# Performance work log

Measured on AMD Instinct MI355X. Metric: run time of the kernel, lower is better.

Reference implementation:

```python
import jax, jax.numpy as jnp
import numpy as np

NEG_BIG = -1e10
LEAKY_ALPHA = 0.2

def setup_inputs() -> dict:
    key = jax.random.key(0)
    k1, k2, k3, k4 = jax.random.split(key, 4)
    B, N, F, H = 8, 2048, 128, 4
    X = jax.random.normal(k1, (B, N, F), dtype=jnp.float32)
    A = jax.random.bernoulli(k2, 0.06, (B, N, N)).astype(jnp.float32)
    A = jnp.maximum(A, jnp.eye(N, dtype=jnp.float32)[None])
    attn_self = jax.random.normal(k3, (H, F), dtype=jnp.float32) * 0.1
    attn_neigh = jax.random.normal(k4, (H, F), dtype=jnp.float32) * 0.1
    return {"X": X, "A": A, "attn_self": attn_self, "attn_neigh": attn_neigh}

def reference(X, A, attn_self, attn_neigh):
    # mode 0, concat reduction, tanh activation (applied per head, as in call_mode0)
    B, N, F = X.shape
    H = attn_self.shape[0]
    a_self = jnp.einsum('bnf,hf->bhn', X, attn_self)   # [B,H,N]
    a_neigh = jnp.einsum('bnf,hf->bhn', X, attn_neigh)  # [B,H,N]
    dense = a_self[:, :, :, None] + a_neigh[:, :, None, :]  # [B,H,N,N]
    dense = jnp.where(dense >= 0, dense, LEAKY_ALPHA * dense)  # leaky relu 0.2
    mask = jnp.where(A == 0.0, NEG_BIG, 0.0)[:, None, :, :]   # [B,1,N,N]
    attn = jax.nn.softmax(dense + mask, axis=-1)               # [B,H,N,N]
    feats = jnp.einsum('bhnm,bmf->bhnf', attn, X)              # [B,H,N,F]
    feats = jnp.tanh(feats)
    # concat heads on feature axis -> [B,N,H*F]
    return feats.transpose(0, 2, 1, 3).reshape(B, N, H * F)
```

## Files before the change

### kernel.cpp

```cpp
#include <hip/hip_runtime.h>
#include <hip/hip_bf16.h>
#include <math.h>

#define N_NODES 2048
#define F_DIM   128
#define H_HEADS 4
#define B_BATCH 8
#define LEAKY   0.2f

typedef float f32x4 __attribute__((ext_vector_type(4)));
typedef float f32x2 __attribute__((ext_vector_type(2)));

__device__ __forceinline__ float tanh_fast(float x) {
    const float e = __expf(2.0f * x);
    return 1.0f - 2.0f / (e + 1.0f);
}

__global__ __launch_bounds__(256) void gat_proj(const float* __restrict__ X,
                                                const float* __restrict__ wS,
                                                const float* __restrict__ wN,
                                                float* __restrict__ aSt,
                                                float* __restrict__ aNt) {
    const int wave = threadIdx.x >> 6;
    const int lane = threadIdx.x & 63;
    const int row  = blockIdx.x * 4 + wave;
    const float* xr = X + (size_t)row * F_DIM;
    const float x0 = xr[lane];
    const float x1 = xr[lane + 64];
    float4 ps4, pn4;
    float* psv = (float*)&ps4;
    float* pnv = (float*)&pn4;
#pragma unroll
    for (int h = 0; h < H_HEADS; ++h) {
        float ps = x0 * wS[h * F_DIM + lane] + x1 * wS[h * F_DIM + 64 + lane];
        float pn = x0 * wN[h * F_DIM + lane] + x1 * wN[h * F_DIM + 64 + lane];
#pragma unroll
        for (int off = 32; off > 0; off >>= 1) {
            ps += __shfl_xor(ps, off);
            pn += __shfl_xor(pn, off);
        }
        psv[h] = ps;
        pnv[h] = pn;
    }
    if (lane == 0) {
        ((float4*)aSt)[row] = ps4;
        ((float4*)aNt)[row] = pn4;
    }
}

__global__ __launch_bounds__(256) void gat_gmax(const float* __restrict__ aNt,
                                                float* __restrict__ gmax) {
    const int b = blockIdx.x;
    const int tid = threadIdx.x;
    const int lane = tid & 63;
    const int wv = tid >> 6;
    __shared__ float4 s_part[4];
    float4 m = make_float4(-1e30f, -1e30f, -1e30f, -1e30f);
    const float4* src = (const float4*)aNt + (size_t)b * N_NODES;
    for (int n = tid; n < N_NODES; n += 256) {
        const float4 v = src[n];
        m.x = fmaxf(m.x, v.x); m.y = fmaxf(m.y, v.y);
        m.z = fmaxf(m.z, v.z); m.w = fmaxf(m.w, v.w);
    }
#pragma unroll
    for (int off = 32; off > 0; off >>= 1) {
        m.x = fmaxf(m.x, __shfl_xor(m.x, off));
        m.y = fmaxf(m.y, __shfl_xor(m.y, off));
        m.z = fmaxf(m.z, __shfl_xor(m.z, off));
        m.w = fmaxf(m.w, __shfl_xor(m.w, off));
    }
    if (lane == 0) s_part[wv] = m;
    __syncthreads();
    if (tid == 0) {
        float4 r = s_part[0];
#pragma unroll
        for (int w = 1; w < 4; ++w) {
            r.x = fmaxf(r.x, s_part[w].x); r.y = fmaxf(r.y, s_part[w].y);
            r.z = fmaxf(r.z, s_part[w].z); r.w = fmaxf(r.w, s_part[w].w);
        }
        ((float4*)gmax)[b] = r;
    }
}

#define FMA16(PV, XV)                                        \
    do {                                                     \
        acc[0][0] = fmaf((PV).x, (XV).x, acc[0][0]);         \
        acc[0][1] = fmaf((PV).x, (XV).y, acc[0][1]);         \
        acc[0][2] = fmaf((PV).x, (XV).z, acc[0][2]);         \
        acc[0][3] = fmaf((PV).x, (XV).w, acc[0][3]);         \
        acc[1][0] = fmaf((PV).y, (XV).x, acc[1][0]);         \
        acc[1][1] = fmaf((PV).y, (XV).y, acc[1][1]);         \
        acc[1][2] = fmaf((PV).y, (XV).z, acc[1][2]);         \
        acc[1][3] = fmaf((PV).y, (XV).w, acc[1][3]);         \
        acc[2][0] = fmaf((PV).z, (XV).x, acc[2][0]);         \
        acc[2][1] = fmaf((PV).z, (XV).y, acc[2][1]);         \
        acc[2][2] = fmaf((PV).z, (XV).z, acc[2][2]);         \
        acc[2][3] = fmaf((PV).z, (XV).w, acc[2][3]);         \
        acc[3][0] = fmaf((PV).w, (XV).x, acc[3][0]);         \
        acc[3][1] = fmaf((PV).w, (XV).y, acc[3][1]);         \
        acc[3][2] = fmaf((PV).w, (XV).z, acc[3][2]);         \
        acc[3][3] = fmaf((PV).w, (XV).w, acc[3][3]);         \
    } while (0)

__global__ __launch_bounds__(256, 6) void gat_main(const float* __restrict__ X,
                                                   const float* __restrict__ A,
                                                   const float* __restrict__ aSt,
                                                   const float* __restrict__ aNt,
                                                   const float* __restrict__ gmax,
                                                   float* __restrict__ out) {
    const int tid = threadIdx.x;
    const int bid = blockIdx.x;
    const int row = ((bid & 7) << 11) | (bid >> 3);
    const int b = row >> 11;
    const int lane = tid & 63;
    const int wv = tid >> 6;

    __shared__ short  s_idx[N_NODES];
    __shared__ float4 s_p4[256];
    __shared__ int    s_off[256];
    __shared__ float  s_red[4 * 512];
    __shared__ int    s_wtot[4];
    __shared__ float  s_M[4];
    __shared__ float  s_sv[4];
    __shared__ float  s_scr[16];

    const f32x4* Arow = (const f32x4*)(A + (size_t)row * N_NODES);
    const f32x4 a0 = __builtin_nontemporal_load(Arow + tid * 2);
    const f32x4 a1 = __builtin_nontemporal_load(Arow + tid * 2 + 1);

    if (tid < 4) {
        const float sv = aSt[(size_t)row * 4 + tid];
        const float g = gmax[b * 4 + tid];
        float v = sv + g;
        v = fmaxf(v, LEAKY * v);
        s_M[tid] = v;
        s_sv[tid] = sv;
    }

    const float av[8] = {a0.x, a0.y, a0.z, a0.w, a1.x, a1.y, a1.z, a1.w};
    int c = 0;
#pragma unroll
    for (int k = 0; k < 8; ++k) c += (av[k] != 0.0f) ? 1 : 0;

    int incl = c;
#pragma unroll
    for (int d = 1; d < 64; d <<= 1) {
        const int u = __shfl_up(incl, d);
        if (lane >= d) incl += u;
    }
    if (lane == 63) s_wtot[wv] = incl;
    __syncthreads();
    int wbase = 0;
#pragma unroll
    for (int w = 0; w < 4; ++w) wbase += (w < wv) ? s_wtot[w] : 0;
    const int cnt = s_wtot[0] + s_wtot[1] + s_wtot[2] + s_wtot[3];
    int pos = wbase + (incl - c);
#pragma unroll
    for (int k = 0; k < 8; ++k) {
        if (av[k] != 0.0f) s_idx[pos++] = (short)(tid * 8 + k);
    }
    __syncthreads();

    float acc[4][4];
#pragma unroll
    for (int h = 0; h < 4; ++h)
#pragma unroll
        for (int fi = 0; fi < 4; ++fi) acc[h][fi] = 0.0f;
    float lsum[4] = {0.0f, 0.0f, 0.0f, 0.0f};

    const int jsub = tid >> 5;
    const int f4 = tid & 31;
    const char* XbB = (const char*)(X + (size_t)b * N_NODES * F_DIM) + (f4 << 4);
    const float4* aNb4 = (const float4*)aNt + (size_t)b * N_NODES;

    for (int base = 0; base < cnt; base += 256) {
        const int clen = min(256, cnt - base);
        if (tid < clen) {
            const int m = s_idx[base + tid];
            const float4 t = aNb4[m];
            const float tv[4] = {t.x, t.y, t.z, t.w};
            float4 p4;
            float* pp = (float*)&p4;
#pragma unroll
            for (int h = 0; h < H_HEADS; ++h) {
                float v = s_sv[h] + tv[h];
                v = fmaxf(v, LEAKY * v);
                const float p = __expf(v - s_M[h]);
                pp[h] = p;
                lsum[h] += p;
            }
            s_p4[tid] = p4;
            s_off[tid] = m << 9;
        }
        __syncthreads();
#pragma unroll 4
        for (int j = jsub; j < clen; j += 8) {
            const float4 pv = s_p4[j];
            const float4 xv = *(const float4*)(XbB + (unsigned)s_off[j]);
            FMA16(pv, xv);
        }
        __syncthreads();
    }

#pragma unroll
    for (int h = 0; h < H_HEADS; ++h) {
        float v = lsum[h];
#pragma unroll
        for (int off = 32; off > 0; off >>= 1) v += __shfl_xor(v, off);
        if (lane == 0) s_scr[wv * 4 + h] = v;
    }
#pragma unroll
    for (int h = 0; h < 4; ++h)
#pragma unroll
        for (int fi = 0; fi < 4; ++fi)
            acc[h][fi] += __shfl_xor(acc[h][fi], 32);
    if (lane < 32) {
        float4* red4 = (float4*)s_red;
#pragma unroll
        for (int h = 0; h < 4; ++h)
            red4[wv * 128 + h * 32 + f4] =
                make_float4(acc[h][0], acc[h][1], acc[h][2], acc[h][3]);
    }
    __syncthreads();

    const int hf = tid * 2;
    const int h = tid >> 6;
    const float l = s_scr[h] + s_scr[4 + h] + s_scr[8 + h] + s_scr[12 + h];
    const float invl = 1.0f / l;
    float v0 = 0.0f, v1 = 0.0f;
#pragma unroll
    for (int w = 0; w < 4; ++w) {
        v0 += s_red[w * 512 + hf];
        v1 += s_red[w * 512 + hf + 1];
    }
    f32x2 o;
    o.x = tanh_fast(v0 * invl);
    o.y = tanh_fast(v1 * invl);
    __builtin_nontemporal_store(o, (f32x2*)&out[(size_t)row * 512 + hf]);
}

extern "C" void kernel_launch(void* const* d_in, const int* in_sizes, int n_in,
                              void* d_out, int out_size, void* d_ws, size_t ws_size,
                              hipStream_t stream) {
    const float* X  = (const float*)d_in[0];
    const float* A  = (const float*)d_in[1];
    const float* wS = (const float*)d_in[2];
    const float* wN = (const float*)d_in[3];
    float* out = (float*)d_out;

    float* aSt = (float*)d_ws;
    float* aNt = aSt + (size_t)B_BATCH * N_NODES * H_HEADS;
    float* gmx = aNt + (size_t)B_BATCH * N_NODES * H_HEADS;

    gat_proj<<<(B_BATCH * N_NODES) / 4, 256, 0, stream>>>(X, wS, wN, aSt, aNt);
    gat_gmax<<<B_BATCH, 256, 0, stream>>>(aNt, gmx);
    gat_main<<<B_BATCH * N_NODES, 256, 0, stream>>>(X, A, aSt, aNt, gmx, out);
}
```

Before: 102.8 us.

## Bit-pack adjacency in a separate pass and compact indices from bitmask in main kernel

Adds a pre-pass that reads the float adjacency and writes a 1-bit-per-edge mask into workspace. The main kernel then reads 256 bytes of mask per row instead of 8 KB of floats, and one wave builds the neighbor index list with popcount, a scan and a find-first-set loop. The pass still reads the whole of A once, so it mainly moves the A read out of the main kernel and adds a launch plus extra mask traffic. A fallback keeps the old kernel when the workspace is too small.

Measured after the change: 111.3 us. 1.08x slower.

```diff
diff --git a/kernel.cpp b/kernel.cpp
--- a/kernel.cpp
+++ b/kernel.cpp
@@ -14,6 +14,25 @@
 __device__ __forceinline__ float tanh_fast(float x) {
     const float e = __expf(2.0f * x);
     return 1.0f - 2.0f / (e + 1.0f);
+}
+
+__global__ __launch_bounds__(256) void gat_bitpack(const float* __restrict__ A,
+                                                   unsigned char* __restrict__ maskb) {
+    const int row = blockIdx.x;
+    const int tid = threadIdx.x;
+    const f32x4* Ar = (const f32x4*)(A + (size_t)row * N_NODES);
+    const f32x4 a0 = __builtin_nontemporal_load(Ar + tid * 2);
+    const f32x4 a1 = __builtin_nontemporal_load(Ar + tid * 2 + 1);
+    unsigned b = 0;
+    b |= (a0.x != 0.0f ? 1u : 0u) << 0;
+    b |= (a0.y != 0.0f ? 1u : 0u) << 1;
+    b |= (a0.z != 0.0f ? 1u : 0u) << 2;
+    b |= (a0.w != 0.0f ? 1u : 0u) << 3;
+    b |= (a1.x != 0.0f ? 1u : 0u) << 4;
+    b |= (a1.y != 0.0f ? 1u : 0u) << 5;
+    b |= (a1.z != 0.0f ? 1u : 0u) << 6;
+    b |= (a1.w != 0.0f ? 1u : 0u) << 7;
+    maskb[(size_t)row * 256 + tid] = (unsigned char)b;
 }
 
 __global__ __launch_bounds__(256) void gat_proj(const float* __restrict__ X,
@@ -103,7 +122,7 @@
     } while (0)
 
 __global__ __launch_bounds__(256, 6) void gat_main(const float* __restrict__ X,
-                                                   const float* __restrict__ A,
+                                                   const unsigned* __restrict__ maskw,
                                                    const float* __restrict__ aSt,
                                                    const float* __restrict__ aNt,
                                                    const float* __restrict__ gmax,
@@ -119,47 +138,43 @@
     __shared__ float4 s_p4[256];
     __shared__ int    s_off[256];
     __shared__ float  s_red[4 * 512];
-    __shared__ int    s_wtot[4];
     __shared__ float  s_M[4];
     __shared__ float  s_sv[4];
     __shared__ float  s_scr[16];
-
-    const f32x4* Arow = (const f32x4*)(A + (size_t)row * N_NODES);
-    const f32x4 a0 = __builtin_nontemporal_load(Arow + tid * 2);
-    const f32x4 a1 = __builtin_nontemporal_load(Arow + tid * 2 + 1);
-
-    if (tid < 4) {
-        const float sv = aSt[(size_t)row * 4 + tid];
-        const float g = gmax[b * 4 + tid];
+    __shared__ int    s_cnt;
+
+    unsigned mw = 0;
+    if (tid < 64) mw = maskw[(size_t)row * 64 + tid];
+
+    if (tid >= 64 && tid < 68) {
+        const int t = tid - 64;
+        const float sv = aSt[(size_t)row * 4 + t];
+        const float g = gmax[b * 4 + t];
         float v = sv + g;
         v = fmaxf(v, LEAKY * v);
-        s_M[tid] = v;
-        s_sv[tid] = sv;
-    }
-
-    const float av[8] = {a0.x, a0.y, a0.z, a0.w, a1.x, a1.y, a1.z, a1.w};
-    int c = 0;
-#pragma unroll
-    for (int k = 0; k < 8; ++k) c += (av[k] != 0.0f) ? 1 : 0;
-
-    int incl = c;
-#pragma unroll
-    for (int d = 1; d < 64; d <<= 1) {
-        const int u = __shfl_up(incl, d);
-        if (lane >= d) incl += u;
-    }
-    if (lane == 63) s_wtot[wv] = incl;
-    __syncthreads();
-    int wbase = 0;
-#pragma unroll
-    for (int w = 0; w < 4; ++w) wbase += (w < wv) ? s_wtot[w] : 0;
-    const int cnt = s_wtot[0] + s_wtot[1] + s_wtot[2] + s_wtot[3];
-    int pos = wbase + (incl - c);
-#pragma unroll
-    for (int k = 0; k < 8; ++k) {
-        if (av[k] != 0.0f) s_idx[pos++] = (short)(tid * 8 + k);
-    }
-    __syncthreads();
+        s_M[t] = v;
+        s_sv[t] = sv;
+    }
+
+    if (tid < 64) {
+        const int c = __popc(mw);
+        int incl = c;
+#pragma unroll
+        for (int d = 1; d < 64; d <<= 1) {
+            const int u = __shfl_up(incl, d);
+            if (lane >= d) incl += u;
+        }
+        if (lane == 63) s_cnt = incl;
+        int p = incl - c;
+        unsigned m = mw;
+        while (m) {
+            const int bpos = __ffs(m) - 1;
+            s_idx[p++] = (short)((lane << 5) + bpos);
+            m &= m - 1;
+        }
+    }
+    __syncthreads();
+    const int cnt = s_cnt;
 
     float acc[4][4];
 #pragma unroll
@@ -239,6 +254,143 @@
     __builtin_nontemporal_store(o, (f32x2*)&out[(size_t)row * 512 + hf]);
 }
 
+__global__ __launch_bounds__(256, 6) void gat_main_fb(const float* __restrict__ X,
+                                                      const float* __restrict__ A,
+                                                      const float* __restrict__ aSt,
+                                                      const float* __restrict__ aNt,
+                                                      const float* __restrict__ gmax,
+                                                      float* __restrict__ out) {
+    const int tid = threadIdx.x;
+    const int bid = blockIdx.x;
+    const int row = ((bid & 7) << 11) | (bid >> 3);
+    const int b = row >> 11;
+    const int lane = tid & 63;
+    const int wv = tid >> 6;
+
+    __shared__ short  s_idx[N_NODES];
+    __shared__ float4 s_p4[256];
+    __shared__ int    s_off[256];
+    __shared__ float  s_red[4 * 512];
+    __shared__ int    s_wtot[4];
+    __shared__ float  s_M[4];
+    __shared__ float  s_sv[4];
+    __shared__ float  s_scr[16];
+
+    const f32x4* Arow = (const f32x4*)(A + (size_t)row * N_NODES);
+    const f32x4 a0 = __builtin_nontemporal_load(Arow + tid * 2);
+    const f32x4 a1 = __builtin_nontemporal_load(Arow + tid * 2 + 1);
+
+    if (tid < 4) {
+        const float sv = aSt[(size_t)row * 4 + tid];
+        const float g = gmax[b * 4 + tid];
+        float v = sv + g;
+        v = fmaxf(v, LEAKY * v);
+        s_M[tid] = v;
+        s_sv[tid] = sv;
+    }
+
+    const float av[8] = {a0.x, a0.y, a0.z, a0.w, a1.x, a1.y, a1.z, a1.w};
+    int c = 0;
+#pragma unroll
+    for (int k = 0; k < 8; ++k) c += (av[k] != 0.0f) ? 1 : 0;
+
+    int incl = c;
+#pragma unroll
+    for (int d = 1; d < 64; d <<= 1) {
+        const int u = __shfl_up(incl, d);
+        if (lane >= d) incl += u;
+    }
+    if (lane == 63) s_wtot[wv] = incl;
+    __syncthreads();
+    int wbase = 0;
+#pragma unroll
+    for (int w = 0; w < 4; ++w) wbase += (w < wv) ? s_wtot[w] : 0;
+    const int cnt = s_wtot[0] + s_wtot[1] + s_wtot[2] + s_wtot[3];
+    int pos = wbase + (incl - c);
+#pragma unroll
+    for (int k = 0; k < 8; ++k) {
+        if (av[k] != 0.0f) s_idx[pos++] = (short)(tid * 8 + k);
+    }
+    __syncthreads();
+
+    float acc[4][4];
+#pragma unroll
+    for (int h = 0; h < 4; ++h)
+#pragma unroll
+        for (int fi = 0; fi < 4; ++fi) acc[h][fi] = 0.0f;
+    float lsum[4] = {0.0f, 0.0f, 0.0f, 0.0f};
+
+    const int jsub = tid >> 5;
+    const int f4 = tid & 31;
+    const char* XbB = (const char*)(X + (size_t)b * N_NODES * F_DIM) + (f4 << 4);
+    const float4* aNb4 = (const float4*)aNt + (size_t)b * N_NODES;
+
+    for (int base = 0; base < cnt; base += 256) {
+        const int clen = min(256, cnt - base);
+        if (tid < clen) {
+            const int m = s_idx[base + tid];
+            const float4 t = aNb4[m];
+            const float tv[4] = {t.x, t.y, t.z, t.w};
+            float4 p4;
+            float* pp = (float*)&p4;
+#pragma unroll
+            for (int h = 0; h < H_HEADS; ++h) {
+                float v = s_sv[h] + tv[h];
+                v = fmaxf(v, LEAKY * v);
+                const float p = __expf(v - s_M[h]);
+                pp[h] = p;
+                lsum[h] += p;
+            }
+            s_p4[tid] = p4;
+            s_off[tid] = m << 9;
+        }
+        __syncthreads();
+#pragma unroll 4
+        for (int j = jsub; j < clen; j += 8) {
+            const float4 pv = s_p4[j];
+            const float4 xv = *(const float4*)(XbB + (unsigned)s_off[j]);
+            FMA16(pv, xv);
+        }
+        __syncthreads();
+    }
+
+#pragma unroll
+    for (int h = 0; h < H_HEADS; ++h) {
+        float v = lsum[h];
+#pragma unroll
+        for (int off = 32; off > 0; off >>= 1) v += __shfl_xor(v, off);
+        if (lane == 0) s_scr[wv * 4 + h] = v;
+    }
+#pragma unroll
+    for (int h = 0; h < 4; ++h)
+#pragma unroll
+        for (int fi = 0; fi < 4; ++fi)
+            acc[h][fi] += __shfl_xor(acc[h][fi], 32);
+    if (lane < 32) {
+        float4* red4 = (float4*)s_red;
+#pragma unroll
+        for (int h = 0; h < 4; ++h)
+            red4[wv * 128 + h * 32 + f4] =
+                make_float4(acc[h][0], acc[h][1], acc[h][2], acc[h][3]);
+    }
+    __syncthreads();
+
+    const int hf = tid * 2;
+    const int h = tid >> 6;
+    const float l = s_scr[h] + s_scr[4 + h] + s_scr[8 + h] + s_scr[12 + h];
+    const float invl = 1.0f / l;
+    float v0 = 0.0f, v1 = 0.0f;
+#pragma unroll
+    for (int w = 0; w < 4; ++w) {
+        v0 += s_red[w * 512 + hf];
+        v1 += s_red[w * 512 + hf + 1];
+    }
+    f32x2 o;
+    o.x = tanh_fast(v0 * invl);
+    o.y = tanh_fast(v1 * invl);
+    __builtin_nontemporal_store(o, (f32x2*)&out[(size_t)row * 512 + hf]);
+}
+
 extern "C" void kernel_launch(void* const* d_in, const int* in_sizes, int n_in,
                               void* d_out, int out_size, void* d_ws, size_t ws_size,
                               hipStream_t stream) {
@@ -251,8 +403,18 @@
     float* aSt = (float*)d_ws;
     float* aNt = aSt + (size_t)B_BATCH * N_NODES * H_HEADS;
     float* gmx = aNt + (size_t)B_BATCH * N_NODES * H_HEADS;
+    unsigned char* maskb = (unsigned char*)(gmx + B_BATCH * H_HEADS);
+
+    const size_t need = ((size_t)B_BATCH * N_NODES * H_HEADS * 2 + B_BATCH * H_HEADS) * 4
+                        + (size_t)B_BATCH * N_NODES * (N_NODES / 8);
 
     gat_proj<<<(B_BATCH * N_NODES) / 4, 256, 0, stream>>>(X, wS, wN, aSt, aNt);
     gat_gmax<<<B_BATCH, 256, 0, stream>>>(aNt, gmx);
-    gat_main<<<B_BATCH * N_NODES, 256, 0, stream>>>(X, A, aSt, aNt, gmx, out);
-}
+    if (ws_size >= need) {
+        gat_bitpack<<<B_BATCH * N_NODES, 256, 0, stream>>>(A, maskb);
+        gat_main<<<B_BATCH * N_NODES, 256, 0, stream>>>(X, (const unsigned*)maskb,
+                                                        aSt, aNt, gmx, out);
+    } else {
+        gat_main_fb<<<B_BATCH * N_NODES, 256, 0, stream>>>(X, A, aSt, aNt, gmx, out);
+    }
+}
```

## Replace sparse gather aggregation with dense bf16 split-precision MFMA kernel

Applied to the files above, without the earlier changes.

Adds a transpose kernel that splits X into bf16 hi/lo parts in a feature-major layout. A new dense kernel computes masked softmax weights for 32 rows by 4 heads per block and runs the attention-times-X product on MFMA 16x16x32 bf16, using hi and lo passes to keep accuracy close to fp32, with double-buffered LDS staging. This replaces the per-row compaction and scalar FMA gather with dense matrix-core work over all N columns, which skips the gather and compaction overhead but computes on zero entries too. The probabilities are rounded to bf16, which adds some error, and the old path stays as a fallback when the workspace is too small.

After: 187.2 us. 1.82x slower.

```diff
diff --git a/kernel.cpp b/kernel.cpp
--- a/kernel.cpp
+++ b/kernel.cpp
@@ -10,17 +10,28 @@
 
 typedef float f32x4 __attribute__((ext_vector_type(4)));
 typedef float f32x2 __attribute__((ext_vector_type(2)));
+typedef short bf16x8 __attribute__((ext_vector_type(8)));
+typedef float f32x4a __attribute__((ext_vector_type(4)));
 
 __device__ __forceinline__ float tanh_fast(float x) {
     const float e = __expf(2.0f * x);
     return 1.0f - 2.0f / (e + 1.0f);
+}
+__device__ __forceinline__ unsigned short f2bf(float x) {
+    unsigned u = __float_as_uint(x);
+    u += 0x7FFFu + ((u >> 16) & 1u);
+    return (unsigned short)(u >> 16);
+}
+__device__ __forceinline__ float bf2f(unsigned short s) {
+    return __uint_as_float(((unsigned)s) << 16);
 }
 
 __global__ __launch_bounds__(256) void gat_proj(const float* __restrict__ X,
                                                 const float* __restrict__ wS,
                                                 const float* __restrict__ wN,
                                                 float* __restrict__ aSt,
-                                                float* __restrict__ aNt) {
+                                                float* __restrict__ aNt,
+                                                float* __restrict__ aNp) {
     const int wave = threadIdx.x >> 6;
     const int lane = threadIdx.x & 63;
     const int row  = blockIdx.x * 4 + wave;
@@ -45,6 +56,10 @@
     if (lane == 0) {
         ((float4*)aSt)[row] = ps4;
         ((float4*)aNt)[row] = pn4;
+        const int bb = row >> 11, nn = row & (N_NODES - 1);
+#pragma unroll
+        for (int h = 0; h < H_HEADS; ++h)
+            aNp[((size_t)(bb * H_HEADS + h)) * N_NODES + nn] = pnv[h];
     }
 }
 
@@ -82,32 +97,172 @@
     }
 }
 
-#define FMA16(PV, XV)                                        \
-    do {                                                     \
-        acc[0][0] = fmaf((PV).x, (XV).x, acc[0][0]);         \
-        acc[0][1] = fmaf((PV).x, (XV).y, acc[0][1]);         \
-        acc[0][2] = fmaf((PV).x, (XV).z, acc[0][2]);         \
-        acc[0][3] = fmaf((PV).x, (XV).w, acc[0][3]);         \
-        acc[1][0] = fmaf((PV).y, (XV).x, acc[1][0]);         \
-        acc[1][1] = fmaf((PV).y, (XV).y, acc[1][1]);         \
-        acc[1][2] = fmaf((PV).y, (XV).z, acc[1][2]);         \
-        acc[1][3] = fmaf((PV).y, (XV).w, acc[1][3]);         \
-        acc[2][0] = fmaf((PV).z, (XV).x, acc[2][0]);         \
-        acc[2][1] = fmaf((PV).z, (XV).y, acc[2][1]);         \
-        acc[2][2] = fmaf((PV).z, (XV).z, acc[2][2]);         \
-        acc[2][3] = fmaf((PV).z, (XV).w, acc[2][3]);         \
-        acc[3][0] = fmaf((PV).w, (XV).x, acc[3][0]);         \
-        acc[3][1] = fmaf((PV).w, (XV).y, acc[3][1]);         \
-        acc[3][2] = fmaf((PV).w, (XV).z, acc[3][2]);         \
-        acc[3][3] = fmaf((PV).w, (XV).w, acc[3][3]);         \
-    } while (0)
-
-__global__ __launch_bounds__(256, 6) void gat_main(const float* __restrict__ X,
-                                                   const float* __restrict__ A,
-                                                   const float* __restrict__ aSt,
-                                                   const float* __restrict__ aNt,
-                                                   const float* __restrict__ gmax,
-                                                   float* __restrict__ out) {
+__global__ __launch_bounds__(256) void gat_xtpose(const float* __restrict__ X,
+                                                  unsigned short* __restrict__ XThi,
+                                                  unsigned short* __restrict__ XTlo) {
+    const int bb = blockIdx.x & 7;
+    const int K0 = (blockIdx.x >> 3) << 7;
+    const int tid = threadIdx.x;
+    __shared__ unsigned short ht[128][136];
+    __shared__ unsigned short lt[128][136];
+    const int f4 = (tid & 31) * 4;
+    for (int kk = tid >> 5; kk < 128; kk += 8) {
+        const float4 x = *(const float4*)&X[((size_t)(bb * N_NODES + K0 + kk)) * F_DIM + f4];
+        const float xs[4] = {x.x, x.y, x.z, x.w};
+#pragma unroll
+        for (int q = 0; q < 4; ++q) {
+            const unsigned short hi = f2bf(xs[q]);
+            ht[f4 + q][kk] = hi;
+            lt[f4 + q][kk] = f2bf(xs[q] - bf2f(hi));
+        }
+    }
+    __syncthreads();
+    const int f = tid >> 1, hf = tid & 1;
+    const size_t obase = ((size_t)(bb * F_DIM + f)) * N_NODES + K0 + hf * 64;
+#pragma unroll
+    for (int c = 0; c < 64; c += 8) {
+        *(bf16x8*)&XThi[obase + c] = *(const bf16x8*)&ht[f][hf * 64 + c];
+        *(bf16x8*)&XTlo[obase + c] = *(const bf16x8*)&lt[f][hf * 64 + c];
+    }
+}
+
+__global__ __launch_bounds__(256, 2) void gat_dense(const float* __restrict__ A,
+                                                    const float* __restrict__ aSt,
+                                                    const float* __restrict__ aNp,
+                                                    const float* __restrict__ gmax,
+                                                    const unsigned short* __restrict__ XThi,
+                                                    const unsigned short* __restrict__ XTlo,
+                                                    float* __restrict__ out) {
+    const int tid = threadIdx.x;
+    const int bid = blockIdx.x;
+    const int b = bid & 7;
+    const int Rbase = (bid >> 3) << 5;
+    const int h = tid >> 6;
+    const int lane = tid & 63;
+    const int mrow = lane & 15;
+    const int kch = lane >> 4;
+
+    __shared__ unsigned short ldsXhi[2][128 * 40];
+    __shared__ unsigned short ldsXlo[2][128 * 40];
+    __shared__ float sml[128];
+
+    const int row0 = b * N_NODES + Rbase + mrow;
+    const float g  = gmax[b * 4 + h];
+    const float aS0 = aSt[(size_t)row0 * 4 + h];
+    const float aS1 = aSt[(size_t)(row0 + 16) * 4 + h];
+    float m0 = aS0 + g; m0 = fmaxf(m0, LEAKY * m0);
+    float m1 = aS1 + g; m1 = fmaxf(m1, LEAKY * m1);
+
+    const float* Ar0 = A + (size_t)row0 * N_NODES;
+    const float* Ar1 = Ar0 + (size_t)16 * N_NODES;
+    const float* aNh = aNp + ((size_t)(b * H_HEADS + h)) * N_NODES;
+
+    const int sf = tid >> 1, shf = tid & 1;
+    const unsigned short* XThiB = XThi + ((size_t)(b * F_DIM + sf)) * N_NODES + shf * 16;
+    const unsigned short* XTloB = XTlo + ((size_t)(b * F_DIM + sf)) * N_NODES + shf * 16;
+    const int sdst = sf * 40 + shf * 16;
+
+    f32x4a acc0[8], acc1[8];
+#pragma unroll
+    for (int ft = 0; ft < 8; ++ft) {
+        acc0[ft] = (f32x4a){0.f, 0.f, 0.f, 0.f};
+        acc1[ft] = (f32x4a){0.f, 0.f, 0.f, 0.f};
+    }
+    float ls0 = 0.f, ls1 = 0.f;
+
+    bf16x8 rh0 = *(const bf16x8*)(XThiB);
+    bf16x8 rh1 = *(const bf16x8*)(XThiB + 8);
+    bf16x8 rl0 = *(const bf16x8*)(XTloB);
+    bf16x8 rl1 = *(const bf16x8*)(XTloB + 8);
+    *(bf16x8*)&ldsXhi[0][sdst] = rh0; *(bf16x8*)&ldsXhi[0][sdst + 8] = rh1;
+    *(bf16x8*)&ldsXlo[0][sdst] = rl0; *(bf16x8*)&ldsXlo[0][sdst + 8] = rl1;
+    __syncthreads();
+
+    const int NS = N_NODES / 32;
+    for (int s = 0; s < NS; ++s) {
+        const int cur = s & 1;
+        const int T = s << 5;
+        if (s + 1 < NS) {
+            const int Tn = T + 32;
+            rh0 = *(const bf16x8*)(XThiB + Tn);
+            rh1 = *(const bf16x8*)(XThiB + Tn + 8);
+            rl0 = *(const bf16x8*)(XTloB + Tn);
+            rl1 = *(const bf16x8*)(XTloB + Tn + 8);
+        }
+        const int ko = T + kch * 8;
+        const f32x4 a0a = __builtin_nontemporal_load((const f32x4*)(Ar0 + ko));
+        const f32x4 a0b = __builtin_nontemporal_load((const f32x4*)(Ar0 + ko + 4));
+        const f32x4 a1a = __builtin_nontemporal_load((const f32x4*)(Ar1 + ko));
+        const f32x4 a1b = __builtin_nontemporal_load((const f32x4*)(Ar1 + ko + 4));
+        const f32x4 ana = *(const f32x4*)(aNh + ko);
+        const f32x4 anb = *(const f32x4*)(aNh + ko + 4);
+        const float a0v[8] = {a0a.x, a0a.y, a0a.z, a0a.w, a0b.x, a0b.y, a0b.z, a0b.w};
+        const float a1v[8] = {a1a.x, a1a.y, a1a.z, a1a.w, a1b.x, a1b.y, a1b.z, a1b.w};
+        const float anv[8] = {ana.x, ana.y, ana.z, ana.w, anb.x, anb.y, anb.z, anb.w};
+        bf16x8 fr0, fr1;
+#pragma unroll
+        for (int j = 0; j < 8; ++j) {
+            float v0 = aS0 + anv[j]; v0 = fmaxf(v0, LEAKY * v0);
+            float v1 = aS1 + anv[j]; v1 = fmaxf(v1, LEAKY * v1);
+            const float p0 = (a0v[j] != 0.f) ? __expf(v0 - m0) : 0.f;
+            const float p1 = (a1v[j] != 0.f) ? __expf(v1 - m1) : 0.f;
+            const unsigned short pb0 = f2bf(p0);
+            const unsigned short pb1 = f2bf(p1);
+            ls0 += bf2f(pb0);
+            ls1 += bf2f(pb1);
+            fr0[j] = (short)pb0;
+            fr1[j] = (short)pb1;
+        }
+#pragma unroll
+        for (int ft = 0; ft < 8; ++ft) {
+            const bf16x8 bh = *(const bf16x8*)&ldsXhi[cur][(ft * 16 + mrow) * 40 + kch * 8];
+            acc0[ft] = __builtin_amdgcn_mfma_f32_16x16x32_bf16(fr0, bh, acc0[ft], 0, 0, 0);
+            acc1[ft] = __builtin_amdgcn_mfma_f32_16x16x32_bf16(fr1, bh, acc1[ft], 0, 0, 0);
+        }
+#pragma unroll
+        for (int ft = 0; ft < 8; ++ft) {
+            const bf16x8 bl = *(const bf16x8*)&ldsXlo[cur][(ft * 16 + mrow) * 40 + kch * 8];
+            acc0[ft] = __builtin_amdgcn_mfma_f32_16x16x32_bf16(fr0, bl, acc0[ft], 0, 0, 0);
+            acc1[ft] = __builtin_amdgcn_mfma_f32_16x16x32_bf16(fr1, bl, acc1[ft], 0, 0, 0);
+        }
+        if (s + 1 < NS) {
+            const int nb = cur ^ 1;
+            *(bf16x8*)&ldsXhi[nb][sdst] = rh0; *(bf16x8*)&ldsXhi[nb][sdst + 8] = rh1;
+            *(bf16x8*)&ldsXlo[nb][sdst] = rl0; *(bf16x8*)&ldsXlo[nb][sdst + 8] = rl1;
+        }
+        __syncthreads();
+    }
+
+    ls0 += __shfl_xor(ls0, 16); ls0 += __shfl_xor(ls0, 32);
+    ls1 += __shfl_xor(ls1, 16); ls1 += __shfl_xor(ls1, 32);
+    if (kch == 0) {
+        sml[h * 32 + mrow] = ls0;
+        sml[h * 32 + 16 + mrow] = ls1;
+    }
+    __syncthreads();
+
+    const size_t outRow0 = (size_t)(b * N_NODES + Rbase);
+#pragma unroll
+    for (int i = 0; i < 4; ++i) {
+        const int r0 = kch * 4 + i;
+        const float inv0 = 1.0f / sml[h * 32 + r0];
+        const float inv1 = 1.0f / sml[h * 32 + 16 + r0];
+        float* o0 = out + (outRow0 + r0) * 512 + h * 128 + mrow;
+        float* o1 = out + (outRow0 + 16 + r0) * 512 + h * 128 + mrow;
+#pragma unroll
+        for (int ft = 0; ft < 8; ++ft) {
+            __builtin_nontemporal_store(tanh_fast(acc0[ft][i] * inv0), o0 + ft * 16);
+            __builtin_nontemporal_store(tanh_fast(acc1[ft][i] * inv1), o1 + ft * 16);
+        }
+    }
+}
+
+__global__ __launch_bounds__(256, 6) void gat_main_fb(const float* __restrict__ X,
+                                                      const float* __restrict__ A,
+                                                      const float* __restrict__ aSt,
+                                                      const float* __restrict__ aNt,
+                                                      const float* __restrict__ gmax,
+                                                      float* __restrict__ out) {
     const int tid = threadIdx.x;
     const int bid = blockIdx.x;
     const int row = ((bid & 7) << 11) | (bid >> 3);
@@ -197,7 +352,13 @@
         for (int j = jsub; j < clen; j += 8) {
             const float4 pv = s_p4[j];
             const float4 xv = *(const float4*)(XbB + (unsigned)s_off[j]);
-            FMA16(pv, xv);
+#pragma unroll
+            for (int h = 0; h < 4; ++h) {
+                acc[h][0] = fmaf(((const float*)&pv)[h], xv.x, acc[h][0]);
+                acc[h][1] = fmaf(((const float*)&pv)[h], xv.y, acc[h][1]);
+                acc[h][2] = fmaf(((const float*)&pv)[h], xv.z, acc[h][2]);
+                acc[h][3] = fmaf(((const float*)&pv)[h], xv.w, acc[h][3]);
+            }
         }
         __syncthreads();
     }
@@ -248,11 +409,24 @@
     const float* wN = (const float*)d_in[3];
     float* out = (float*)d_out;
 
+    const size_t nBNH = (size_t)B_BATCH * N_NODES * H_HEADS;
     float* aSt = (float*)d_ws;
-    float* aNt = aSt + (size_t)B_BATCH * N_NODES * H_HEADS;
-    float* gmx = aNt + (size_t)B_BATCH * N_NODES * H_HEADS;
-
-    gat_proj<<<(B_BATCH * N_NODES) / 4, 256, 0, stream>>>(X, wS, wN, aSt, aNt);
+    float* aNt = aSt + nBNH;
+    float* gmx = aNt + nBNH;
+    float* aNp = gmx + B_BATCH * H_HEADS;
+    unsigned short* XThi = (unsigned short*)(aNp + nBNH);
+    unsigned short* XTlo = XThi + (size_t)B_BATCH * F_DIM * N_NODES;
+
+    const size_t need = (nBNH * 3 + B_BATCH * H_HEADS) * 4
+                        + (size_t)B_BATCH * F_DIM * N_NODES * 2 * 2;
+
+    gat_proj<<<(B_BATCH * N_NODES) / 4, 256, 0, stream>>>(X, wS, wN, aSt, aNt, aNp);
     gat_gmax<<<B_BATCH, 256, 0, stream>>>(aNt, gmx);
-    gat_main<<<B_BATCH * N_NODES, 256, 0, stream>>>(X, A, aSt, aNt, gmx, out);
-}
+    if (ws_size >= need) {
+        gat_xtpose<<<B_BATCH * (N_NODES / 128), 256, 0, stream>>>(X, XThi, XTlo);
+        gat_dense<<<B_BATCH * (N_NODES / 32), 256, 0, stream>>>(A, aSt, aNp, gmx,
+                                                                XThi, XTlo, out);
+    } else {
+        gat_main_fb<<<B_BATCH * N_NODES, 256, 0, stream>>>(X, A, aSt, aNt, gmx, out);
+    }
+}
```
